# Kernel tuning notes

Measured on AMD Instinct MI355X. Metric: run time of the kernel, lower is better.

## Reference

```python
import jax, jax.numpy as jnp
import numpy as np

IMG = 224
PS = 2
C_IN = 3
EMBED = 768
BATCH = 256
SLICES = IMG // 2            # 112
L = 2 * (SLICES // PS)       # 112 levels
K = IMG * PS                 # 448 gathered (a,b) pairs per level
D_IN = K * C_IN              # 1344


def _build_levels(n=IMG, slices=SLICES, ps=PS):
    """Replicates LUnraveling index construction (natural order; set() in the
    original only permutes within a level, which is equivalent up to a fixed
    permutation of weight columns for random init)."""
    a_list, b_list = [], []
    ar = np.arange(n)
    for i in range(slices // ps):
        cols = range(i * ps, (i + 1) * ps)
        # 'up' level: pairs (j, col) for j in range(n), concatenated over ps cols
        a_list.append(np.concatenate([ar for _ in cols]))
        b_list.append(np.concatenate([np.full(n, c) for c in cols]))
        # 'right' level: pairs (n - slices + col, j) for j in range(n)
        a_list.append(np.concatenate([np.full(n, n - slices + c) for c in cols]))
        b_list.append(np.concatenate([ar for _ in cols]))
    return (np.stack(a_list).astype(np.int32), np.stack(b_list).astype(np.int32))


def setup_inputs() -> dict:
    key = jax.random.key(0)
    k1, k2, k3 = jax.random.split(key, 3)
    x = jax.random.normal(k1, (BATCH, C_IN, IMG, IMG), dtype=jnp.float32)
    W = jax.random.normal(k2, (EMBED, D_IN), dtype=jnp.float32) * (1.0 / np.sqrt(D_IN))
    b = jax.random.normal(k3, (EMBED,), dtype=jnp.float32) * 0.01
    a_np, b_np = _build_levels()
    return {"x": x, "W": W, "b": b,
            "a_idx": jnp.asarray(a_np), "b_idx": jnp.asarray(b_np)}


def reference(x, W, b, a_idx, b_idx):
    B = x.shape[0]
    # gather: x[:, :, a, b] with (L,K) index arrays -> (B, C, L, K)
    g = x[:, :, a_idx, b_idx]
    # per-level flatten(1) in torch flattens (C, K) C-major -> (B, L, C*K)
    g = jnp.transpose(g, (0, 2, 1, 3)).reshape(B, L, C_IN * K)
    # shared linear projection per level token
    tokens = jnp.einsum('bld,ed->ble', g, W) + b
    return tokens  # (B, L, EMBED); norm is Identity (norm_layer=None)
```

## Files before the change

kernel.cpp:

```cpp
#include <hip/hip_runtime.h>
#include <stdint.h>


#define IMG   224
#define NLEV  112
#define CIN   3
#define DIN   1344
#define EMB   768
#define BATCH 256
#define MTOT  28672

#define BM    128
#define BN    128
#define BK    64
#define LDP   72

#define AS1 __attribute__((address_space(1)))
#define AS3 __attribute__((address_space(3)))

typedef __attribute__((ext_vector_type(8))) short   short8;
typedef __attribute__((ext_vector_type(4))) float   floatx4;

__device__ __forceinline__ unsigned short f2bf(float f) {
    unsigned u = __float_as_uint(f);
    unsigned r = (u + 0x7fffu + ((u >> 16) & 1u)) >> 16;
    return (unsigned short)r;
}
__device__ __forceinline__ float bf2f(unsigned short s) {
    return __uint_as_float(((unsigned)s) << 16);
}
__device__ __forceinline__ unsigned pack2(float a, float b) {
    return (unsigned)f2bf(a) | ((unsigned)f2bf(b) << 16);
}

__global__ void detect_dtype(const unsigned short* __restrict__ W, int* flag) {
    __shared__ int s;
    if (threadIdx.x == 0) s = 0;
    __syncthreads();
    int bad = 0;
    for (int k = threadIdx.x; k < 4096; k += 256) {
        unsigned v = (unsigned)W[2 * k] & 0x7FFFu;
        if (v >= 0x4000u) bad = 1;
    }
    if (bad) atomicOr(&s, 1);
    __syncthreads();
    if (threadIdx.x == 0) *flag = s;
}

__global__ __launch_bounds__(256)
void pack_w(const void* __restrict__ Wv, const void* __restrict__ Bv,
            unsigned short* __restrict__ Wb, float* __restrict__ Bf,
            const int* __restrict__ flag)
{
    const bool F32 = (*flag != 0);
    const int idx = blockIdx.x * 256 + threadIdx.x;
    if (F32) {
        const float4* s = (const float4*)((const float*)Wv + (size_t)idx * 8);
        float4 x0 = s[0], x1 = s[1];
        uint4 o;
        o.x = pack2(x0.x, x0.y); o.y = pack2(x0.z, x0.w);
        o.z = pack2(x1.x, x1.y); o.w = pack2(x1.z, x1.w);
        ((uint4*)Wb)[idx] = o;
    } else {
        ((uint4*)Wb)[idx] = ((const uint4*)Wv)[idx];
    }
    if (idx < EMB)
        Bf[idx] = F32 ? ((const float*)Bv)[idx]
                      : bf2f(((const unsigned short*)Bv)[idx]);
}

__global__ __launch_bounds__(256)
void pack_g_rows(const void* __restrict__ Xv, unsigned short* __restrict__ Gc,
                 int b0, const int* __restrict__ flag)
{
    const bool F32 = (*flag != 0);
    const int tid = threadIdx.x;
    const int bl  = blockIdx.x;
    const int c   = blockIdx.y;
    const size_t plane = ((size_t)(b0 + bl) * CIN + c) * (size_t)(IMG * IMG);
    unsigned short* Grow = Gc + (size_t)bl * NLEV * DIN + (size_t)c * 448;

    if (F32) {
        const float* src = (const float*)Xv + plane + (size_t)NLEV * IMG;
        for (int v = tid; v < 3136; v += 256) {
            const int i  = v / 56;
            const int kk = (v - i * 56) * 8;
            const float4* s = (const float4*)(src + (size_t)v * 8);
            float4 x0 = s[0], x1 = s[1];
            uint4 o;
            o.x = pack2(x0.x, x0.y); o.y = pack2(x0.z, x0.w);
            o.z = pack2(x1.x, x1.y); o.w = pack2(x1.z, x1.w);
            *(uint4*)(Grow + (size_t)(2 * i + 1) * DIN + kk) = o;
        }
    } else {
        const unsigned short* src = (const unsigned short*)Xv + plane + (size_t)NLEV * IMG;
        for (int v = tid; v < 3136; v += 256) {
            const int i  = v / 56;
            const int kk = (v - i * 56) * 8;
            *(uint4*)(Grow + (size_t)(2 * i + 1) * DIN + kk) =
                *(const uint4*)(src + (size_t)v * 8);
        }
    }
}

__global__ __launch_bounds__(256)
void pack_g_cols(const void* __restrict__ Xv, unsigned short* __restrict__ Gc,
                 int b0, const int* __restrict__ flag)
{
    const bool F32 = (*flag != 0);
    __shared__ __align__(16) unsigned short lds[IMG * 116];

    const int tid = threadIdx.x;
    const int bl  = blockIdx.x;
    const int c   = blockIdx.y;
    const size_t plane = ((size_t)(b0 + bl) * CIN + c) * (size_t)(IMG * IMG);
    unsigned short* Grow = Gc + (size_t)bl * NLEV * DIN + (size_t)c * 448;

    for (int v = tid; v < 3136; v += 256) {
        const int r  = v / 14;
        const int vv = v - r * 14;
        if (F32) {
            const float4* s = (const float4*)((const float*)Xv + plane
                              + (size_t)r * IMG + (size_t)vv * 8);
            float4 x0 = s[0], x1 = s[1];
            uint2 o0, o1;
            o0.x = pack2(x0.x, x0.y); o0.y = pack2(x0.z, x0.w);
            o1.x = pack2(x1.x, x1.y); o1.y = pack2(x1.z, x1.w);
            *(uint2*)&lds[r * 116 + vv * 8]     = o0;
            *(uint2*)&lds[r * 116 + vv * 8 + 4] = o1;
        } else {
            const uint2* s = (const uint2*)((const unsigned short*)Xv + plane
                              + (size_t)r * IMG + (size_t)vv * 8);
            *(uint2*)&lds[r * 116 + vv * 8]     = s[0];
            *(uint2*)&lds[r * 116 + vv * 8 + 4] = s[1];
        }
    }
    __syncthreads();

    for (int idx = tid; idx < 56 * 28; idx += 256) {
        const int pr = idx / 28;
        const int t  = idx - pr * 28;
        const int r0 = t * 8;
        unsigned v[8];
        #pragma unroll
        for (int j = 0; j < 8; j++)
            v[j] = *(const unsigned*)&lds[(r0 + j) * 116 + 2 * pr];
        uint4 lo, hi;
        lo.x = (v[0] & 0xFFFFu) | (v[1] << 16);
        lo.y = (v[2] & 0xFFFFu) | (v[3] << 16);
        lo.z = (v[4] & 0xFFFFu) | (v[5] << 16);
        lo.w = (v[6] & 0xFFFFu) | (v[7] << 16);
        hi.x = (v[0] >> 16) | (v[1] & 0xFFFF0000u);
        hi.y = (v[2] >> 16) | (v[3] & 0xFFFF0000u);
        hi.z = (v[4] >> 16) | (v[5] & 0xFFFF0000u);
        hi.w = (v[6] >> 16) | (v[7] & 0xFFFF0000u);
        unsigned short* dst = Grow + (size_t)(2 * pr) * DIN + r0;
        *(uint4*)dst         = lo;
        *(uint4*)(dst + IMG) = hi;
    }
}

__global__ __launch_bounds__(256)
void gemm_packed(const unsigned short* __restrict__ G,
                 const unsigned short* __restrict__ Wb,
                 const float* __restrict__ Bf,
                 float* __restrict__ Out)
{
    __shared__ __align__(16) unsigned short As[128 * 64];
    __shared__ __align__(16) unsigned short Bs[128 * 64];

    const int tid  = threadIdx.x;
    const int wave = tid >> 6;
    const int lane = tid & 63;

    const int bid = blockIdx.x;
    const int nwg = gridDim.x;
    const int q = nwg >> 3, r = nwg & 7;
    const int xcd = bid & 7, s = bid >> 3;
    const int lid = (xcd < r ? xcd * (q + 1) : r * (q + 1) + (xcd - r) * q) + s;
    const int mT = lid / 6;
    const int nT = lid - mT * 6;
    const int mBase = mT * 128;
    const int nBase = nT * 128;

    const int wm   = wave >> 1, wn = wave & 1;
    const int lrow = lane & 15;
    const int kq   = (lane >> 4) << 3;

    floatx4 acc[4][4];
    #pragma unroll
    for (int i = 0; i < 4; i++)
        #pragma unroll
        for (int j = 0; j < 4; j++)
            acc[i][j] = (floatx4){0.f, 0.f, 0.f, 0.f};

    const unsigned short* gaP[4];
    const unsigned short* gbP[4];
    unsigned ldsOff[4];
    #pragma unroll
    for (int i = 0; i < 4; i++) {
        const int idx = (i * 4 + wave) * 64 + lane;
        const int row = idx >> 3, k8 = idx & 7;
        gaP[i] = G  + (size_t)(mBase + row) * DIN + k8 * 8;
        gbP[i] = Wb + (size_t)(nBase + row) * DIN + k8 * 8;
        ldsOff[i] = (unsigned)((i * 4 + wave) * 512);
    }

    for (int kt = 0; kt < DIN; kt += 64) {
        #pragma unroll
        for (int i = 0; i < 4; i++) {
            __builtin_amdgcn_global_load_lds(
                (const AS1 void*)(gaP[i] + kt),
                (AS3 void*)(As + ldsOff[i]), 16, 0, 0);
            __builtin_amdgcn_global_load_lds(
                (const AS1 void*)(gbP[i] + kt),
                (AS3 void*)(Bs + ldsOff[i]), 16, 0, 0);
        }
        __syncthreads();

        #pragma unroll
        for (int k0 = 0; k0 < 64; k0 += 32) {
            short8 af[4], bfv[4];
            #pragma unroll
            for (int mi = 0; mi < 4; mi++)
                af[mi] = *(const short8*)&As[(wm * 64 + mi * 16 + lrow) * 64 + k0 + kq];
            #pragma unroll
            for (int ni = 0; ni < 4; ni++)
                bfv[ni] = *(const short8*)&Bs[(wn * 64 + ni * 16 + lrow) * 64 + k0 + kq];
            #pragma unroll
            for (int mi = 0; mi < 4; mi++)
                #pragma unroll
                for (int ni = 0; ni < 4; ni++)
                    acc[mi][ni] = __builtin_amdgcn_mfma_f32_16x16x32_bf16(
                        af[mi], bfv[ni], acc[mi][ni], 0, 0, 0);
        }
        __syncthreads();
    }

    const int quad = lane >> 4;
    #pragma unroll
    for (int ni = 0; ni < 4; ni++) {
        const int col = nBase + wn * 64 + ni * 16 + lrow;
        const float bv = Bf[col];
        #pragma unroll
        for (int mi = 0; mi < 4; mi++) {
            const int rbase = mBase + wm * 64 + mi * 16 + quad * 4;
            floatx4 a = acc[mi][ni];
            Out[(size_t)(rbase + 0) * EMB + col] = a[0] + bv;
            Out[(size_t)(rbase + 1) * EMB + col] = a[1] + bv;
            Out[(size_t)(rbase + 2) * EMB + col] = a[2] + bv;
            Out[(size_t)(rbase + 3) * EMB + col] = a[3] + bv;
        }
    }
}

template<bool F32>
__global__ __launch_bounds__(256, 2)
void lfreq_fused_gemm(const void* __restrict__ Xv,
                      const void* __restrict__ Wv,
                      const void* __restrict__ Bv,
                      const int* __restrict__ Aidx,
                      const int* __restrict__ Bidx,
                      float* __restrict__ Out,
                      const int* __restrict__ flag)
{
    if (*flag != (F32 ? 1 : 0)) return;

    __shared__ __align__(16) unsigned short As[BM][LDP];
    __shared__ __align__(16) unsigned short Bs[BN][LDP];

    const int tid   = threadIdx.x;
    const int wave  = tid >> 6;
    const int lane  = tid & 63;
    const int mBase = blockIdx.x * BM;
    const int nBase = blockIdx.y * BN;

    const int srow  = tid >> 1;
    const int shalf = tid & 1;
    const int am = mBase + srow;
    const int bb = am / NLEV;
    const int ll = am - bb * NLEV;

    floatx4 acc[4][4];
    #pragma unroll
    for (int i = 0; i < 4; i++)
        #pragma unroll
        for (int jj = 0; jj < 4; jj++)
            acc[i][jj] = (floatx4){0.f, 0.f, 0.f, 0.f};

    const int wm   = wave >> 1;
    const int wn   = wave & 1;
    const int lrow = lane & 15;
    const int kq   = (lane >> 4) << 3;

    for (int kt = 0; kt < DIN; kt += BK) {
        {
            const int koff = kt + shalf * 32;
            uint4* dst = (uint4*)&Bs[srow][shalf * 32];
            if (F32) {
                const float4* g = (const float4*)((const float*)Wv
                                + (size_t)(nBase + srow) * DIN + koff);
                #pragma unroll
                for (int q = 0; q < 4; q++) {
                    float4 v0 = g[2*q], v1 = g[2*q+1];
                    uint4 o;
                    o.x = pack2(v0.x, v0.y); o.y = pack2(v0.z, v0.w);
                    o.z = pack2(v1.x, v1.y); o.w = pack2(v1.z, v1.w);
                    dst[q] = o;
                }
            } else {
                const uint4* g = (const uint4*)((const unsigned short*)Wv
                               + (size_t)(nBase + srow) * DIN + koff);
                #pragma unroll
                for (int q = 0; q < 4; q++) dst[q] = g[q];
            }
        }
        {
            const int d0  = kt + shalf * 32;
            const int c   = (d0 >= 896) ? 2 : (d0 >= 448 ? 1 : 0);
            const int kk0 = d0 - c * 448;
            const int4* ap = (const int4*)(Aidx + ll * 448 + kk0);
            const int4* bp = (const int4*)(Bidx + ll * 448 + kk0);
            unsigned* du = (unsigned*)&As[srow][shalf * 32];
            if (F32) {
                const float* plane = (const float*)Xv
                    + (size_t)bb * (CIN * IMG * IMG) + (size_t)c * (IMG * IMG);
                #pragma unroll
                for (int q = 0; q < 8; q++) {
                    int4 av = ap[q], bv = bp[q];
                    du[2*q+0] = pack2(plane[av.x * IMG + bv.x], plane[av.y * IMG + bv.y]);
                    du[2*q+1] = pack2(plane[av.z * IMG + bv.z], plane[av.w * IMG + bv.w]);
                }
            } else {
                const unsigned short* plane = (const unsigned short*)Xv
                    + (size_t)bb * (CIN * IMG * IMG) + (size_t)c * (IMG * IMG);
                #pragma unroll
                for (int q = 0; q < 8; q++) {
                    int4 av = ap[q], bv = bp[q];
                    unsigned e0 = plane[av.x * IMG + bv.x];
                    unsigned e1 = plane[av.y * IMG + bv.y];
                    unsigned e2 = plane[av.z * IMG + bv.z];
                    unsigned e3 = plane[av.w * IMG + bv.w];
                    du[2*q+0] = e0 | (e1 << 16);
                    du[2*q+1] = e2 | (e3 << 16);
                }
            }
        }
        __syncthreads();

        #pragma unroll
        for (int k0 = 0; k0 < BK; k0 += 32) {
            short8 af[4], bfv[4];
            #pragma unroll
            for (int mi = 0; mi < 4; mi++)
                af[mi] = *(const short8*)&As[wm*64 + mi*16 + lrow][k0 + kq];
            #pragma unroll
            for (int ni = 0; ni < 4; ni++)
                bfv[ni] = *(const short8*)&Bs[wn*64 + ni*16 + lrow][k0 + kq];
            #pragma unroll
            for (int mi = 0; mi < 4; mi++)
                #pragma unroll
                for (int ni = 0; ni < 4; ni++)
                    acc[mi][ni] = __builtin_amdgcn_mfma_f32_16x16x32_bf16(
                        af[mi], bfv[ni], acc[mi][ni], 0, 0, 0);
        }
        __syncthreads();
    }

    const int quad = lane >> 4;
    #pragma unroll
    for (int ni = 0; ni < 4; ni++) {
        const int col = nBase + wn*64 + ni*16 + lrow;
        const float bv = F32 ? ((const float*)Bv)[col]
                             : bf2f(((const unsigned short*)Bv)[col]);
        #pragma unroll
        for (int mi = 0; mi < 4; mi++) {
            const int rbase = mBase + wm*64 + mi*16 + quad*4;
            floatx4 a = acc[mi][ni];
            Out[(size_t)(rbase+0)*EMB + col] = a[0] + bv;
            Out[(size_t)(rbase+1)*EMB + col] = a[1] + bv;
            Out[(size_t)(rbase+2)*EMB + col] = a[2] + bv;
            Out[(size_t)(rbase+3)*EMB + col] = a[3] + bv;
        }
    }
}

extern "C" void kernel_launch(void* const* d_in, const int* in_sizes, int n_in,
                              void* d_out, int out_size, void* d_ws, size_t ws_size,
                              hipStream_t stream) {
    const void* X    = d_in[0];
    const void* Wt   = d_in[1];
    const void* Bias = d_in[2];
    const int*  Ai   = (const int*)d_in[3];
    const int*  Bi   = (const int*)d_in[4];
    float* Out = (float*)d_out;

    char* ws  = (char*)d_ws;
    int* flag = (int*)ws;

    detect_dtype<<<dim3(1), dim3(256), 0, stream>>>((const unsigned short*)Wt, flag);

    float* Bf          = (float*)(ws + 256);
    unsigned short* Wb = (unsigned short*)(ws + 4096);
    const size_t gOff  = 4096 + (size_t)EMB * DIN * 2;
    unsigned short* Gc = (unsigned short*)(ws + gOff);

    int CHB = 0;
    const int cand[6] = {256, 128, 64, 32, 16, 8};
    for (int t = 0; t < 6; t++) {
        if (gOff + (size_t)cand[t] * NLEV * DIN * 2 <= ws_size) { CHB = cand[t]; break; }
    }

    if (CHB == 0) {
        dim3 grid(MTOT / BM, EMB / BN);
        lfreq_fused_gemm<false><<<grid, dim3(256), 0, stream>>>(X, Wt, Bias, Ai, Bi, Out, flag);
        lfreq_fused_gemm<true ><<<grid, dim3(256), 0, stream>>>(X, Wt, Bias, Ai, Bi, Out, flag);
        return;
    }

    pack_w<<<dim3(504), dim3(256), 0, stream>>>(Wt, Bias, Wb, Bf, flag);

    for (int b0 = 0; b0 < BATCH; b0 += CHB) {
        dim3 pgrid(CHB, CIN);
        pack_g_rows<<<pgrid, dim3(256), 0, stream>>>(X, Gc, b0, flag);
        pack_g_cols<<<pgrid, dim3(256), 0, stream>>>(X, Gc, b0, flag);
        dim3 ggrid(CHB * NLEV / 128 * 6);
        gemm_packed<<<ggrid, dim3(256), 0, stream>>>(Gc, Wb, Bf,
                                                     Out + (size_t)b0 * NLEV * EMB);
    }
}
```

Measured before the change: 363.9 us.

## Double-buffer GEMM LDS tiles with XOR swizzle and merge gather pack kernels

```diff
diff --git a/kernel.cpp b/kernel.cpp
--- a/kernel.cpp
+++ b/kernel.cpp
@@ -9,6 +9,7 @@
 #define EMB   768
 #define BATCH 256
 #define MTOT  28672
+#define NT    21
 
 #define BM    128
 #define BN    128
@@ -70,10 +71,12 @@
 }
 
 __global__ __launch_bounds__(256)
-void pack_g_rows(const void* __restrict__ Xv, unsigned short* __restrict__ Gc,
-                 int b0, const int* __restrict__ flag)
+void pack_g(const void* __restrict__ Xv, unsigned short* __restrict__ Gc,
+            int b0, const int* __restrict__ flag)
 {
     const bool F32 = (*flag != 0);
+    __shared__ __align__(16) unsigned short lds[IMG * 128];
+
     const int tid = threadIdx.x;
     const int bl  = blockIdx.x;
     const int c   = blockIdx.y;
@@ -101,62 +104,49 @@
                 *(const uint4*)(src + (size_t)v * 8);
         }
     }
-}
-
-__global__ __launch_bounds__(256)
-void pack_g_cols(const void* __restrict__ Xv, unsigned short* __restrict__ Gc,
-                 int b0, const int* __restrict__ flag)
-{
-    const bool F32 = (*flag != 0);
-    __shared__ __align__(16) unsigned short lds[IMG * 116];
-
-    const int tid = threadIdx.x;
-    const int bl  = blockIdx.x;
-    const int c   = blockIdx.y;
-    const size_t plane = ((size_t)(b0 + bl) * CIN + c) * (size_t)(IMG * IMG);
-    unsigned short* Grow = Gc + (size_t)bl * NLEV * DIN + (size_t)c * 448;
 
     for (int v = tid; v < 3136; v += 256) {
         const int r  = v / 14;
         const int vv = v - r * 14;
+        const int key = (r >> 3) & 15;
+        uint2 o0, o1;
         if (F32) {
             const float4* s = (const float4*)((const float*)Xv + plane
                               + (size_t)r * IMG + (size_t)vv * 8);
             float4 x0 = s[0], x1 = s[1];
-            uint2 o0, o1;
             o0.x = pack2(x0.x, x0.y); o0.y = pack2(x0.z, x0.w);
             o1.x = pack2(x1.x, x1.y); o1.y = pack2(x1.z, x1.w);
-            *(uint2*)&lds[r * 116 + vv * 8]     = o0;
-            *(uint2*)&lds[r * 116 + vv * 8 + 4] = o1;
         } else {
             const uint2* s = (const uint2*)((const unsigned short*)Xv + plane
                               + (size_t)r * IMG + (size_t)vv * 8);
-            *(uint2*)&lds[r * 116 + vv * 8]     = s[0];
-            *(uint2*)&lds[r * 116 + vv * 8 + 4] = s[1];
-        }
+            o0 = s[0]; o1 = s[1];
+        }
+        *(uint2*)&lds[r * 128 + ((2 * vv)     ^ key) * 4] = o0;
+        *(uint2*)&lds[r * 128 + ((2 * vv + 1) ^ key) * 4] = o1;
     }
     __syncthreads();
 
-    for (int idx = tid; idx < 56 * 28; idx += 256) {
-        const int pr = idx / 28;
-        const int t  = idx - pr * 28;
-        const int r0 = t * 8;
-        unsigned v[8];
-        #pragma unroll
-        for (int j = 0; j < 8; j++)
-            v[j] = *(const unsigned*)&lds[(r0 + j) * 116 + 2 * pr];
-        uint4 lo, hi;
-        lo.x = (v[0] & 0xFFFFu) | (v[1] << 16);
-        lo.y = (v[2] & 0xFFFFu) | (v[3] << 16);
-        lo.z = (v[4] & 0xFFFFu) | (v[5] << 16);
-        lo.w = (v[6] & 0xFFFFu) | (v[7] << 16);
-        hi.x = (v[0] >> 16) | (v[1] & 0xFFFF0000u);
-        hi.y = (v[2] >> 16) | (v[3] & 0xFFFF0000u);
-        hi.z = (v[4] >> 16) | (v[5] & 0xFFFF0000u);
-        hi.w = (v[6] >> 16) | (v[7] & 0xFFFF0000u);
-        unsigned short* dst = Grow + (size_t)(2 * pr) * DIN + r0;
-        *(uint4*)dst         = lo;
-        *(uint4*)(dst + IMG) = hi;
+    for (int idx = tid; idx < 56 * 56; idx += 256) {
+        const int pr   = idx / 56;
+        const int j    = idx - pr * 56;
+        const int half = j / 28;
+        const int r0   = (j - half * 28) * 8;
+        const int qb   = pr >> 1;
+        const int sh   = (pr & 1) * 2;
+        unsigned short h[8];
+        #pragma unroll
+        for (int m = 0; m < 8; m++) {
+            const int r = r0 + m;
+            const unsigned v = *(const unsigned*)
+                &lds[r * 128 + (qb ^ ((r >> 3) & 15)) * 4 + sh];
+            h[m] = half ? (unsigned short)(v >> 16) : (unsigned short)(v & 0xFFFFu);
+        }
+        uint4 o;
+        o.x = (unsigned)h[0] | ((unsigned)h[1] << 16);
+        o.y = (unsigned)h[2] | ((unsigned)h[3] << 16);
+        o.z = (unsigned)h[4] | ((unsigned)h[5] << 16);
+        o.w = (unsigned)h[6] | ((unsigned)h[7] << 16);
+        *(uint4*)(Grow + (size_t)(2 * pr) * DIN + half * IMG + r0) = o;
     }
 }
 
@@ -166,8 +156,8 @@
                  const float* __restrict__ Bf,
                  float* __restrict__ Out)
 {
-    __shared__ __align__(16) unsigned short As[128 * 64];
-    __shared__ __align__(16) unsigned short Bs[128 * 64];
+    __shared__ __align__(16) unsigned short As[2][128 * 64];
+    __shared__ __align__(16) unsigned short Bs[2][128 * 64];
 
     const int tid  = threadIdx.x;
     const int wave = tid >> 6;
@@ -186,6 +176,7 @@
     const int wm   = wave >> 1, wn = wave & 1;
     const int lrow = lane & 15;
     const int kq   = (lane >> 4) << 3;
+    const int swz  = (lrow & 7) << 3;
 
     floatx4 acc[4][4];
     #pragma unroll
@@ -201,40 +192,59 @@
     for (int i = 0; i < 4; i++) {
         const int idx = (i * 4 + wave) * 64 + lane;
         const int row = idx >> 3, k8 = idx & 7;
-        gaP[i] = G  + (size_t)(mBase + row) * DIN + k8 * 8;
-        gbP[i] = Wb + (size_t)(nBase + row) * DIN + k8 * 8;
+        const int jc  = k8 ^ (row & 7);
+        gaP[i] = G  + (size_t)(mBase + row) * DIN + jc * 8;
+        gbP[i] = Wb + (size_t)(nBase + row) * DIN + jc * 8;
         ldsOff[i] = (unsigned)((i * 4 + wave) * 512);
     }
 
-    for (int kt = 0; kt < DIN; kt += 64) {
-        #pragma unroll
-        for (int i = 0; i < 4; i++) {
-            __builtin_amdgcn_global_load_lds(
-                (const AS1 void*)(gaP[i] + kt),
-                (AS3 void*)(As + ldsOff[i]), 16, 0, 0);
-            __builtin_amdgcn_global_load_lds(
-                (const AS1 void*)(gbP[i] + kt),
-                (AS3 void*)(Bs + ldsOff[i]), 16, 0, 0);
-        }
-        __syncthreads();
-
+    #pragma unroll
+    for (int i = 0; i < 4; i++) {
+        __builtin_amdgcn_global_load_lds((const AS1 void*)(gaP[i]),
+                                         (AS3 void*)(&As[0][0] + ldsOff[i]), 16, 0, 0);
+        __builtin_amdgcn_global_load_lds((const AS1 void*)(gbP[i]),
+                                         (AS3 void*)(&Bs[0][0] + ldsOff[i]), 16, 0, 0);
+    }
+    __syncthreads();
+
+    int cur = 0;
+    for (int t = 0; t < NT; ++t) {
+        if (t < NT - 1) {
+            const int kt = (t + 1) * 64;
+            #pragma unroll
+            for (int i = 0; i < 4; i++) {
+                __builtin_amdgcn_global_load_lds(
+                    (const AS1 void*)(gaP[i] + kt),
+                    (AS3 void*)(&As[cur ^ 1][0] + ldsOff[i]), 16, 0, 0);
+                __builtin_amdgcn_global_load_lds(
+                    (const AS1 void*)(gbP[i] + kt),
+                    (AS3 void*)(&Bs[cur ^ 1][0] + ldsOff[i]), 16, 0, 0);
+            }
+        }
+        const unsigned short* Ab = &As[cur][0];
+        const unsigned short* Bb = &Bs[cur][0];
         #pragma unroll
         for (int k0 = 0; k0 < 64; k0 += 32) {
             short8 af[4], bfv[4];
             #pragma unroll
             for (int mi = 0; mi < 4; mi++)
-                af[mi] = *(const short8*)&As[(wm * 64 + mi * 16 + lrow) * 64 + k0 + kq];
+                af[mi] = *(const short8*)&Ab[(wm * 64 + mi * 16 + lrow) * 64
+                                             + ((k0 + kq) ^ swz)];
             #pragma unroll
             for (int ni = 0; ni < 4; ni++)
-                bfv[ni] = *(const short8*)&Bs[(wn * 64 + ni * 16 + lrow) * 64 + k0 + kq];
+                bfv[ni] = *(const short8*)&Bb[(wn * 64 + ni * 16 + lrow) * 64
+                                              + ((k0 + kq) ^ swz)];
+            __builtin_amdgcn_s_setprio(1);
             #pragma unroll
             for (int mi = 0; mi < 4; mi++)
                 #pragma unroll
                 for (int ni = 0; ni < 4; ni++)
                     acc[mi][ni] = __builtin_amdgcn_mfma_f32_16x16x32_bf16(
                         af[mi], bfv[ni], acc[mi][ni], 0, 0, 0);
+            __builtin_amdgcn_s_setprio(0);
         }
         __syncthreads();
+        cur ^= 1;
     }
 
     const int quad = lane >> 4;
@@ -422,8 +432,7 @@
 
     for (int b0 = 0; b0 < BATCH; b0 += CHB) {
         dim3 pgrid(CHB, CIN);
-        pack_g_rows<<<pgrid, dim3(256), 0, stream>>>(X, Gc, b0, flag);
-        pack_g_cols<<<pgrid, dim3(256), 0, stream>>>(X, Gc, b0, flag);
+        pack_g<<<pgrid, dim3(256), 0, stream>>>(X, Gc, b0, flag);
         dim3 ggrid(CHB * NLEV / 128 * 6);
         gemm_packed<<<ggrid, dim3(256), 0, stream>>>(Gc, Wb, Bf,
                                                      Out + (size_t)b0 * NLEV * EMB);
```

Result: faster. 346.4 us (-4.8%).
